# Kernel tuning notes

Measured on AMD Instinct MI355X. Metric: run time of the kernel, lower is better.

The kernel has to match this reference:

```python
import jax, jax.numpy as jnp
import numpy as np

N, E, R = 50000, 320000, 3
IN, HID, OUT = 768, 256, 64
NEG_SLOPE = 0.2


def _rgat_conv(x, src, dst, edge_type, W, q, k, bias):
    # x: [N, HID]; W: [R, HID, HID]; q,k: [HID, 1]; bias: [HID]
    n = x.shape[0]
    xw = jnp.einsum('nc,rco->rno', x, W)          # [R, N, HID] per-relation transform
    out_i = xw[edge_type, dst]                      # [E, HID] transformed target feats
    out_j = xw[edge_type, src]                      # [E, HID] transformed source feats
    alpha = jax.nn.leaky_relu(out_i @ q + out_j @ k, NEG_SLOPE)  # [E, 1]
    # across-relation segment softmax over destination nodes (PyG softmax semantics)
    m = jax.ops.segment_max(alpha, dst, num_segments=n)          # [N, 1]
    ea = jnp.exp(alpha - m[dst])
    denom = jax.ops.segment_sum(ea, dst, num_segments=n)         # [N, 1]
    a = ea / (denom[dst] + 1e-16)                                # [E, 1]
    out = jax.ops.segment_sum(a * out_j, dst, num_segments=n)    # [N, HID]
    return out + bias


def setup_inputs() -> dict:
    key = jax.random.key(0)
    ks = jax.random.split(key, 16)
    g = lambda k, shape, fan: (jax.random.normal(k, shape, jnp.float32) / np.float32(np.sqrt(fan)))
    return {
        'x': jax.random.normal(ks[0], (N, IN), jnp.float32),
        'edge_index': jax.random.randint(ks[1], (2, E), 0, N),
        'edge_type': jax.random.randint(ks[2], (E,), 0, R),
        'w_in': g(ks[3], (IN, HID), IN), 'b_in': jnp.zeros((HID,), jnp.float32),
        'conv1_w': g(ks[4], (R, HID, HID), HID),
        'conv1_q': g(ks[5], (HID, 1), HID),
        'conv1_k': g(ks[6], (HID, 1), HID),
        'conv1_b': jnp.zeros((HID,), jnp.float32),
        'conv2_w': g(ks[7], (R, HID, HID), HID),
        'conv2_q': g(ks[8], (HID, 1), HID),
        'conv2_k': g(ks[9], (HID, 1), HID),
        'conv2_b': jnp.zeros((HID,), jnp.float32),
        'w_out': g(ks[10], (HID, OUT), HID), 'b_out': jnp.zeros((OUT,), jnp.float32),
        'w_cls': g(ks[11], (OUT, 2), OUT), 'b_cls': jnp.zeros((2,), jnp.float32),
    }


def reference(x, edge_index, edge_type, w_in, b_in,
              conv1_w, conv1_q, conv1_k, conv1_b,
              conv2_w, conv2_q, conv2_k, conv2_b,
              w_out, b_out, w_cls, b_cls):
    src, dst = edge_index[0], edge_index[1]
    h = jax.nn.relu(x @ w_in + b_in)                                  # [N, HID]
    h = _rgat_conv(h, src, dst, edge_type, conv1_w, conv1_q, conv1_k, conv1_b)
    h = _rgat_conv(h, src, dst, edge_type, conv2_w, conv2_q, conv2_k, conv2_b)
    h = jax.nn.relu(h @ w_out + b_out)                                # [N, OUT]
    return h @ w_cls + b_cls                                          # [N, 2]
```

## Files before the change

### kernel.cpp

```cpp
#include <hip/hip_runtime.h>
#include <hip/hip_bf16.h>

#define RG86_NN 50000
#define RG86_NE 320000
#define RG86_NR 3
#define RG86_DIN 768
#define RG86_HID 256
#define RG86_OUT 64

typedef __bf16 rg_bv8 __attribute__((ext_vector_type(8)));
typedef short rg_sv8 __attribute__((ext_vector_type(8)));
typedef float rg_fv4 __attribute__((ext_vector_type(4)));
typedef unsigned int rg_u32;

static __device__ float rg_b2f(unsigned short u) {
  return __uint_as_float(((unsigned int)u) << 16);
}
static __device__ unsigned short rg_f2b(float f) {
  unsigned int u = __float_as_uint(f);
  u += 0x7FFFu + ((u >> 16) & 1u);
  return (unsigned short)(u >> 16);
}

static __device__ __forceinline__ void rg_gl16(const void* g, void* lds_wave_base) {
  __builtin_amdgcn_global_load_lds(
      (const __attribute__((address_space(1))) rg_u32*)(unsigned long long)(uintptr_t)g,
      (__attribute__((address_space(3))) rg_u32*)(unsigned int)(uintptr_t)lds_wave_base,
      16, 0, 0);
}

__global__ void RGATModel_86371792322702_kernel() {}

__global__ void rg_castT(const float* in, unsigned short* out, int rows, int cols) {
  int i = blockIdx.x * 256 + threadIdx.x;
  if (i < rows * cols) {
    int r = i / cols, c = i % cols;
    out[(size_t)c * rows + r] = rg_f2b(in[i]);
  }
}

__global__ void rg_castT3(const float* in, unsigned short* out) {
  int i = blockIdx.x * 256 + threadIdx.x;
  if (i < RG86_NR * RG86_HID * RG86_HID) {
    int r = i >> 16, j = i & 65535;
    int row = j >> 8, col = j & 255;
    out[(r << 16) + (col << 8) + row] = rg_f2b(in[i]);
  }
}

__global__ void rg_wqk(const float* W, const float* q, const float* k,
                       float* wq, float* wk) {
  int lane = threadIdx.x & 63;
  int p = blockIdx.x * 4 + (threadIdx.x >> 6);
  if (p >= RG86_NR * RG86_HID) return;
  const float* wr = W + (size_t)p * RG86_HID;
  float qv = 0.f, kv = 0.f;
  for (int j = lane; j < RG86_HID; j += 64) {
    float w = wr[j];
    qv += w * q[j];
    kv += w * k[j];
  }
  for (int o = 32; o >= 1; o >>= 1) { qv += __shfl_xor(qv, o); kv += __shfl_xor(kv, o); }
  if (lane == 0) { wq[p] = qv; wk[p] = kv; }
}

__global__ void rg_qk2(const unsigned short* h, const float* wq, const float* wk,
                       float* qd, float* kd) {
  int lane = threadIdx.x & 63;
  int n = blockIdx.x * 4 + (threadIdx.x >> 6);
  if (n >= RG86_NN) return;
  ushort4 hv = *(const ushort4*)(h + (size_t)n * RG86_HID + lane * 4);
  float h0 = rg_b2f(hv.x), h1 = rg_b2f(hv.y), h2 = rg_b2f(hv.z), h3 = rg_b2f(hv.w);
  float acc[6];
#pragma unroll
  for (int r = 0; r < RG86_NR; r++) {
    const float* wqr = wq + r * RG86_HID + lane * 4;
    const float* wkr = wk + r * RG86_HID + lane * 4;
    acc[r] = h0 * wqr[0] + h1 * wqr[1] + h2 * wqr[2] + h3 * wqr[3];
    acc[3 + r] = h0 * wkr[0] + h1 * wkr[1] + h2 * wkr[2] + h3 * wkr[3];
  }
#pragma unroll
  for (int j = 0; j < 6; j++)
    for (int o = 32; o >= 1; o >>= 1) acc[j] += __shfl_xor(acc[j], o);
  if (lane == 0) {
#pragma unroll
    for (int r = 0; r < RG86_NR; r++) {
      qd[r * RG86_NN + n] = acc[r];
      kd[r * RG86_NN + n] = acc[3 + r];
    }
  }
}

__global__ __launch_bounds__(256) void rg_gemm2(
    const unsigned short* A, const unsigned short* Bt, const float* bias,
    unsigned short* C, int M, int N, int K, int relu, int split) {
  __shared__ unsigned short sA[128 * 64];
  __shared__ unsigned short sB[64 * 64];
  int tid = threadIdx.x;
  int wv = tid >> 6, lane = tid & 63;
  int nwg = gridDim.x;
  int q = nwg >> 3, rres = nwg & 7;
  int xcd = blockIdx.x & 7, jj = blockIdx.x >> 3;
  int wg = (xcd < rres ? xcd * (q + 1) : rres * (q + 1) + (xcd - rres) * q) + jj;
  int ntiles = N >> 6;
  int mt = wg / ntiles, nt = wg - mt * ntiles;
  int m0 = mt * 128, n0 = nt * 64;
  int frow = lane & 15, fhi = lane >> 4;
  rg_fv4 acc[2][4] = {};
  for (int k0 = 0; k0 < K; k0 += 64) {
#pragma unroll
    for (int i = 0; i < 4; i++) {
      int idx = i * 256 + tid;
      int r = idx >> 3, s = idx & 7;
      int gr = m0 + r;
      if (gr >= M) gr = M - 1;
      const unsigned short* gp = A + (size_t)gr * K + k0 + ((s ^ (r & 7)) << 3);
      rg_gl16(gp, (char*)sA + (size_t)(i * 256 + wv * 64) * 16);
    }
#pragma unroll
    for (int i = 0; i < 2; i++) {
      int idx = i * 256 + tid;
      int r = idx >> 3, s = idx & 7;
      const unsigned short* gp = Bt + (size_t)(n0 + r) * K + k0 + ((s ^ (r & 7)) << 3);
      rg_gl16(gp, (char*)sB + (size_t)(i * 256 + wv * 64) * 16);
    }
    __syncthreads();
#pragma unroll
    for (int ks = 0; ks < 2; ks++) {
      rg_bv8 af[2], bf[4];
#pragma unroll
      for (int mf = 0; mf < 2; mf++) {
        int r = wv * 32 + mf * 16 + frow;
        int slot = (ks * 4 + fhi) ^ (r & 7);
        af[mf] = *(const rg_bv8*)((const char*)sA + r * 128 + slot * 16);
      }
#pragma unroll
      for (int nf = 0; nf < 4; nf++) {
        int r = nf * 16 + frow;
        int slot = (ks * 4 + fhi) ^ (r & 7);
        bf[nf] = *(const rg_bv8*)((const char*)sB + r * 128 + slot * 16);
      }
#pragma unroll
      for (int mf = 0; mf < 2; mf++)
#pragma unroll
        for (int nf = 0; nf < 4; nf++)
          acc[mf][nf] = __builtin_amdgcn_mfma_f32_16x16x32_bf16(af[mf], bf[nf],
                                                                acc[mf][nf], 0, 0, 0);
    }
    __syncthreads();
  }
#pragma unroll
  for (int mf = 0; mf < 2; mf++) {
#pragma unroll
    for (int nf = 0; nf < 4; nf++) {
      int col = n0 + nf * 16 + frow;
      float bv = bias ? bias[col] : 0.f;
#pragma unroll
      for (int r = 0; r < 4; r++) {
        int row = m0 + wv * 32 + mf * 16 + fhi * 4 + r;
        if (row < M) {
          float v = acc[mf][nf][r] + bv;
          if (relu && v < 0.f) v = 0.f;
          if (split)
            C[((size_t)(col >> 8) * RG86_NN + row) * 256 + (col & 255)] = rg_f2b(v);
          else
            C[(size_t)row * N + col] = rg_f2b(v);
        }
      }
    }
  }
}

__global__ __launch_bounds__(256) void rg_gemm2f(
    const float* A, const unsigned short* Bt, const float* bias,
    unsigned short* C, int M, int N, int K, int relu) {
  __shared__ unsigned short sA[128 * 64];
  __shared__ unsigned short sB[64 * 64];
  int tid = threadIdx.x;
  int wv = tid >> 6, lane = tid & 63;
  int nwg = gridDim.x;
  int q = nwg >> 3, rres = nwg & 7;
  int xcd = blockIdx.x & 7, jj = blockIdx.x >> 3;
  int wg = (xcd < rres ? xcd * (q + 1) : rres * (q + 1) + (xcd - rres) * q) + jj;
  int ntiles = N >> 6;
  int mt = wg / ntiles, nt = wg - mt * ntiles;
  int m0 = mt * 128, n0 = nt * 64;
  int frow = lane & 15, fhi = lane >> 4;
  rg_fv4 acc[2][4] = {};
  for (int k0 = 0; k0 < K; k0 += 64) {
#pragma unroll
    for (int i = 0; i < 2; i++) {
      int idx = i * 256 + tid;
      int r = idx >> 3, s = idx & 7;
      const unsigned short* gp = Bt + (size_t)(n0 + r) * K + k0 + ((s ^ (r & 7)) << 3);
      rg_gl16(gp, (char*)sB + (size_t)(i * 256 + wv * 64) * 16);
    }
    float4 fa[4][2];
#pragma unroll
    for (int i = 0; i < 4; i++) {
      int idx = i * 256 + tid;
      int r = idx >> 3, s = idx & 7;
      int gr = m0 + r;
      if (gr >= M) gr = M - 1;
      const float* gp = A + (size_t)gr * K + k0 + ((s ^ (r & 7)) << 3);
      fa[i][0] = *(const float4*)gp;
      fa[i][1] = *(const float4*)(gp + 4);
    }
#pragma unroll
    for (int i = 0; i < 4; i++) {
      int idx = i * 256 + tid;
      rg_sv8 bvv;
      bvv[0] = (short)rg_f2b(fa[i][0].x);
      bvv[1] = (short)rg_f2b(fa[i][0].y);
      bvv[2] = (short)rg_f2b(fa[i][0].z);
      bvv[3] = (short)rg_f2b(fa[i][0].w);
      bvv[4] = (short)rg_f2b(fa[i][1].x);
      bvv[5] = (short)rg_f2b(fa[i][1].y);
      bvv[6] = (short)rg_f2b(fa[i][1].z);
      bvv[7] = (short)rg_f2b(fa[i][1].w);
      *(rg_sv8*)((char*)sA + (size_t)idx * 16) = bvv;
    }
    __syncthreads();
#pragma unroll
    for (int ks = 0; ks < 2; ks++) {
      rg_bv8 af[2], bf[4];
#pragma unroll
      for (int mf = 0; mf < 2; mf++) {
        int r = wv * 32 + mf * 16 + frow;
        int slot = (ks * 4 + fhi) ^ (r & 7);
        af[mf] = *(const rg_bv8*)((const char*)sA + r * 128 + slot * 16);
      }
#pragma unroll
      for (int nf = 0; nf < 4; nf++) {
        int r = nf * 16 + frow;
        int slot = (ks * 4 + fhi) ^ (r & 7);
        bf[nf] = *(const rg_bv8*)((const char*)sB + r * 128 + slot * 16);
      }
#pragma unroll
      for (int mf = 0; mf < 2; mf++)
#pragma unroll
        for (int nf = 0; nf < 4; nf++)
          acc[mf][nf] = __builtin_amdgcn_mfma_f32_16x16x32_bf16(af[mf], bf[nf],
                                                                acc[mf][nf], 0, 0, 0);
    }
    __syncthreads();
  }
#pragma unroll
  for (int mf = 0; mf < 2; mf++) {
#pragma unroll
    for (int nf = 0; nf < 4; nf++) {
      int col = n0 + nf * 16 + frow;
      float bv = bias ? bias[col] : 0.f;
#pragma unroll
      for (int r = 0; r < 4; r++) {
        int row = m0 + wv * 32 + mf * 16 + fhi * 4 + r;
        if (row < M) {
          float v = acc[mf][nf][r] + bv;
          if (relu && v < 0.f) v = 0.f;
          C[(size_t)row * N + col] = rg_f2b(v);
        }
      }
    }
  }
}

__global__ void rg_hist(const int* d, int* counts) {
  int e = blockIdx.x * 256 + threadIdx.x;
  if (e < RG86_NE) atomicAdd(&counts[d[e]], 1);
}

__global__ void rg_scan1(const int* counts, int* tmp, int* bsum, int n) {
  int b = blockIdx.x, t = threadIdx.x;
  int base = b * 1024 + t * 4;
  int v0 = 0, v1 = 0, v2 = 0, v3 = 0;
  if (base + 3 < n) {
    int4 v = *(const int4*)(counts + base);
    v0 = v.x; v1 = v.y; v2 = v.z; v3 = v.w;
  } else {
    if (base + 0 < n) v0 = counts[base + 0];
    if (base + 1 < n) v1 = counts[base + 1];
    if (base + 2 < n) v2 = counts[base + 2];
    if (base + 3 < n) v3 = counts[base + 3];
  }
  int tsum = v0 + v1 + v2 + v3;
  int lane = t & 63, wave = t >> 6;
  int s = tsum;
  for (int off = 1; off < 64; off <<= 1) {
    int u = __shfl_up(s, off);
    if (lane >= off) s += u;
  }
  __shared__ int wsum[4];
  if (lane == 63) wsum[wave] = s;
  __syncthreads();
  int woff = 0;
  for (int w = 0; w < wave; w++) woff += wsum[w];
  int excl = woff + s - tsum;
  int e0 = excl, e1 = e0 + v0, e2 = e1 + v1, e3 = e2 + v2;
  if (base + 3 < n) {
    *(int4*)(tmp + base) = make_int4(e0, e1, e2, e3);
  } else {
    if (base + 0 < n) tmp[base + 0] = e0;
    if (base + 1 < n) tmp[base + 1] = e1;
    if (base + 2 < n) tmp[base + 2] = e2;
    if (base + 3 < n) tmp[base + 3] = e3;
  }
  if (t == 255) bsum[b] = woff + s;
}

__global__ void rg_scan2(int* bsum, int* rowptr, int nb, int n) {
  int lane = threadIdx.x;
  int v = (lane < nb) ? bsum[lane] : 0;
  int s = v;
  for (int off = 1; off < 64; off <<= 1) {
    int u = __shfl_up(s, off);
    if (lane >= off) s += u;
  }
  if (lane < nb) bsum[lane] = s - v;
  if (lane == 63) rowptr[n] = s;
}

__global__ void rg_scan3(const int* bsum, int* rowptr, int* cursor, int n) {
  int b = blockIdx.x, t = threadIdx.x;
  int base = b * 1024 + t * 4;
  int off = bsum[b];
  if (base + 3 < n) {
    int4 v = *(const int4*)(cursor + base);
    int4 o = make_int4(v.x + off, v.y + off, v.z + off, v.w + off);
    *(int4*)(rowptr + base) = o;
    *(int4*)(cursor + base) = o;
  } else {
    for (int j = 0; j < 4; j++)
      if (base + j < n) {
        int o = cursor[base + j] + off;
        rowptr[base + j] = o;
        cursor[base + j] = o;
      }
  }
}

__global__ void rg_scatter(const int* d, int* cursor, int* perm) {
  int e = blockIdx.x * 256 + threadIdx.x;
  if (e < RG86_NE) perm[atomicAdd(&cursor[d[e]], 1)] = e;
}

__global__ void rg_edge(const int* perm, const int* src, const int* dst,
                        const int* et, const float* qd, const float* kd,
                        float* alphap, int* srcrel) {
  int i = blockIdx.x * 256 + threadIdx.x;
  if (i >= RG86_NE) return;
  int e = perm[i];
  int t = et[e], sv = src[e], dv = dst[e];
  float al = qd[t * RG86_NN + dv] + kd[t * RG86_NN + sv];
  al = al > 0.f ? al : 0.2f * al;
  alphap[i] = al;
  srcrel[i] = t * RG86_NN + sv;
}

__global__ void rg_agg(const int* rowptr, const float* alphap, const int* srcrel,
                       const unsigned short* xw, const float* bias,
                       unsigned short* out) {
  __shared__ float sw[4][64];
  __shared__ int ssrc[4][64];
  int lane = threadIdx.x & 63;
  int wv = threadIdx.x >> 6;
  int node = blockIdx.x * 4 + wv;
  if (node >= RG86_NN) return;
  int s0 = rowptr[node], s1 = rowptr[node + 1];
  int c0 = lane * 4;
  float a0 = 0.f, a1 = 0.f, a2 = 0.f, a3 = 0.f;
  if (s1 > s0) {
    float m = -1e30f;
    for (int bs = s0; bs < s1; bs += 64) {
      int i = bs + lane;
      float al = (i < s1) ? alphap[i] : -1e30f;
      m = fmaxf(m, al);
    }
    for (int o = 32; o >= 1; o >>= 1) m = fmaxf(m, __shfl_xor(m, o));
    float den = 0.f;
    for (int bs = s0; bs < s1; bs += 64) {
      int i = bs + lane;
      if (i < s1) den += __expf(alphap[i] - m);
    }
    for (int o = 32; o >= 1; o >>= 1) den += __shfl_xor(den, o);
    float inv = 1.f / (den + 1e-16f);
    for (int bs = s0; bs < s1; bs += 64) {
      int i = bs + lane;
      int nch = s1 - bs; if (nch > 64) nch = 64;
      float w = 0.f; int sr = 0;
      if (i < s1) { w = __expf(alphap[i] - m) * inv; sr = srcrel[i]; }
      sw[wv][lane] = w;
      ssrc[wv][lane] = sr;
#pragma unroll 4
      for (int j = 0; j < nch; j++) {
        float wj = sw[wv][j];
        ushort4 v = *(const ushort4*)(xw + (size_t)ssrc[wv][j] * RG86_HID + c0);
        a0 += wj * rg_b2f(v.x);
        a1 += wj * rg_b2f(v.y);
        a2 += wj * rg_b2f(v.z);
        a3 += wj * rg_b2f(v.w);
      }
    }
  }
  unsigned short* op = out + (size_t)node * RG86_HID + c0;
  op[0] = rg_f2b(a0 + bias[c0 + 0]);
  op[1] = rg_f2b(a1 + bias[c0 + 1]);
  op[2] = rg_f2b(a2 + bias[c0 + 2]);
  op[3] = rg_f2b(a3 + bias[c0 + 3]);
}

__global__ void rg_cls(const unsigned short* h4, const float* wc, const float* bc,
                       float* out) {
  int n = blockIdx.x * 256 + threadIdx.x;
  if (n >= RG86_NN) return;
  float a0 = bc[0], a1 = bc[1];
  const unsigned short* hr = h4 + (size_t)n * RG86_OUT;
  for (int j = 0; j < RG86_OUT; j++) {
    float h = rg_b2f(hr[j]);
    a0 += h * wc[j * 2 + 0];
    a1 += h * wc[j * 2 + 1];
  }
  out[n * 2 + 0] = a0;
  out[n * 2 + 1] = a1;
}

extern "C" void kernel_launch(void* const* d_in, const int* in_sizes, int n_in,
                              void* d_out, int out_size, void* d_ws, size_t ws_size,
                              hipStream_t stream) {
  (void)in_sizes; (void)n_in; (void)out_size;
  const float* x = (const float*)d_in[0];
  const int* ei = (const int*)d_in[1];
  const int* etp = (const int*)d_in[2];
  const float* w_in = (const float*)d_in[3];
  const float* b_in = (const float*)d_in[4];
  const float* c1w = (const float*)d_in[5];
  const float* c1q = (const float*)d_in[6];
  const float* c1k = (const float*)d_in[7];
  const float* c1b = (const float*)d_in[8];
  const float* c2w = (const float*)d_in[9];
  const float* c2q = (const float*)d_in[10];
  const float* c2k = (const float*)d_in[11];
  const float* c2b = (const float*)d_in[12];
  const float* w_out = (const float*)d_in[13];
  const float* b_out = (const float*)d_in[14];
  const float* w_cls = (const float*)d_in[15];
  const float* b_cls = (const float*)d_in[16];
  const int* esrc = ei;
  const int* edst = ei + RG86_NE;

  char* base = (char*)d_ws;
  size_t off = 0;
  unsigned short* xw = (unsigned short*)(base + off);
  off += (size_t)RG86_NR * RG86_NN * RG86_HID * 2;
  unsigned short* h1b = (unsigned short*)(base + off); off += (size_t)RG86_NN * RG86_HID * 2;
  unsigned short* h2b = (unsigned short*)(base + off); off += (size_t)RG86_NN * RG86_HID * 2;
  unsigned short* h4b = (unsigned short*)(base + off); off += (size_t)RG86_NN * RG86_OUT * 2;
  unsigned short* w_inT = (unsigned short*)(base + off); off += (size_t)RG86_DIN * RG86_HID * 2;
  unsigned short* c1wT = (unsigned short*)(base + off); off += (size_t)RG86_NR * RG86_HID * RG86_HID * 2;
  unsigned short* c2wT = (unsigned short*)(base + off); off += (size_t)RG86_NR * RG86_HID * RG86_HID * 2;
  unsigned short* w_outT = (unsigned short*)(base + off); off += (size_t)RG86_HID * RG86_OUT * 2;
  float* qd = (float*)(base + off); off += (size_t)RG86_NR * RG86_NN * 4;
  float* kd = (float*)(base + off); off += (size_t)RG86_NR * RG86_NN * 4;
  float* wq1 = (float*)(base + off); off += (size_t)RG86_NR * RG86_HID * 4;
  float* wk1 = (float*)(base + off); off += (size_t)RG86_NR * RG86_HID * 4;
  float* wq2 = (float*)(base + off); off += (size_t)RG86_NR * RG86_HID * 4;
  float* wk2 = (float*)(base + off); off += (size_t)RG86_NR * RG86_HID * 4;
  int* counts = (int*)(base + off); off += (size_t)RG86_NN * 4;
  int* rowptr = (int*)(base + off); off += (size_t)(RG86_NN + 4) * 4;
  int* cursor = (int*)(base + off); off += (size_t)RG86_NN * 4;
  int* perm = (int*)(base + off); off += (size_t)RG86_NE * 4;
  int* bsum = (int*)(base + off); off += (size_t)64 * 4;
  float* alphap = (float*)(base + off); off += (size_t)RG86_NE * 4;
  int* srcrel = (int*)(base + off); off += (size_t)RG86_NE * 4;
  if (off > ws_size) return;

  int mt128 = (RG86_NN + 127) / 128;
  int nsb = (RG86_NN + 1023) / 1024;

  rg_castT<<<(RG86_DIN * RG86_HID + 255) / 256, 256, 0, stream>>>(
      w_in, w_inT, RG86_DIN, RG86_HID);
  rg_castT3<<<(RG86_NR * RG86_HID * RG86_HID + 255) / 256, 256, 0, stream>>>(c1w, c1wT);
  rg_castT3<<<(RG86_NR * RG86_HID * RG86_HID + 255) / 256, 256, 0, stream>>>(c2w, c2wT);
  rg_castT<<<(RG86_HID * RG86_OUT + 255) / 256, 256, 0, stream>>>(
      w_out, w_outT, RG86_HID, RG86_OUT);
  rg_wqk<<<(RG86_NR * RG86_HID + 3) / 4, 256, 0, stream>>>(c1w, c1q, c1k, wq1, wk1);
  rg_wqk<<<(RG86_NR * RG86_HID + 3) / 4, 256, 0, stream>>>(c2w, c2q, c2k, wq2, wk2);

  rg_gemm2f<<<mt128 * 4, 256, 0, stream>>>(x, w_inT, b_in, h1b,
                                           RG86_NN, RG86_HID, RG86_DIN, 1);

  hipMemsetAsync(counts, 0, (size_t)RG86_NN * 4, stream);
  rg_hist<<<(RG86_NE + 255) / 256, 256, 0, stream>>>(edst, counts);
  rg_scan1<<<nsb, 256, 0, stream>>>(counts, cursor, bsum, RG86_NN);
  rg_scan2<<<1, 64, 0, stream>>>(bsum, rowptr, nsb, RG86_NN);
  rg_scan3<<<nsb, 256, 0, stream>>>(bsum, rowptr, cursor, RG86_NN);
  rg_scatter<<<(RG86_NE + 255) / 256, 256, 0, stream>>>(edst, cursor, perm);

  rg_gemm2<<<mt128 * 12, 256, 0, stream>>>(h1b, c1wT, (const float*)0, xw,
                                           RG86_NN, RG86_NR * RG86_HID, RG86_HID, 0, 1);
  rg_qk2<<<(RG86_NN + 3) / 4, 256, 0, stream>>>(h1b, wq1, wk1, qd, kd);
  rg_edge<<<(RG86_NE + 255) / 256, 256, 0, stream>>>(perm, esrc, edst, etp, qd, kd,
                                                     alphap, srcrel);
  rg_agg<<<(RG86_NN + 3) / 4, 256, 0, stream>>>(rowptr, alphap, srcrel,
                                                xw, c1b, h2b);

  rg_gemm2<<<mt128 * 12, 256, 0, stream>>>(h2b, c2wT, (const float*)0, xw,
                                           RG86_NN, RG86_NR * RG86_HID, RG86_HID, 0, 1);
  rg_qk2<<<(RG86_NN + 3) / 4, 256, 0, stream>>>(h2b, wq2, wk2, qd, kd);
  rg_edge<<<(RG86_NE + 255) / 256, 256, 0, stream>>>(perm, esrc, edst, etp, qd, kd,
                                                     alphap, srcrel);
  rg_agg<<<(RG86_NN + 3) / 4, 256, 0, stream>>>(rowptr, alphap, srcrel,
                                                xw, c2b, h1b);

  rg_gemm2<<<mt128, 256, 0, stream>>>(h1b, w_outT, b_out, h4b,
                                      RG86_NN, RG86_OUT, RG86_HID, 1, 0);

  rg_cls<<<(RG86_NN + 255) / 256, 256, 0, stream>>>(h4b, w_cls, b_cls, (float*)d_out);
}
```

Before: 622.7 us.

## Widen GEMM tiles to 128x128, pre-cast input to bf16, fuse classifier into output GEMM

The GEMM N-tile grows from 64 to 128 columns, so each A tile loaded into LDS feeds twice as many MFMAs and the grid shrinks by half. The fp32 input x is first cast to bf16 in a separate vectorized pass, so the input GEMM can use the async global_load_lds path instead of converting inside its loop. The final w_out GEMM now applies relu and the 64x2 classifier in its epilogue with a shuffle reduction, removing the h4 buffer and the rg_cls kernel. The cost is an extra full read and write of x for the cast, plus more accumulator registers that may reduce occupancy.

```diff
diff --git a/kernel.cpp b/kernel.cpp
--- a/kernel.cpp
+++ b/kernel.cpp
@@ -30,6 +30,15 @@
 }
 
 __global__ void RGATModel_86371792322702_kernel() {}
+
+__global__ void rg_cast(const float* in, unsigned short* out, int n) {
+  int i = (blockIdx.x * 256 + threadIdx.x) * 4;
+  if (i < n) {
+    float4 v = *(const float4*)(in + i);
+    ushort4 o = make_ushort4(rg_f2b(v.x), rg_f2b(v.y), rg_f2b(v.z), rg_f2b(v.w));
+    *(ushort4*)(out + i) = o;
+  }
+}
 
 __global__ void rg_castT(const float* in, unsigned short* out, int rows, int cols) {
   int i = blockIdx.x * 256 + threadIdx.x;
@@ -91,22 +100,22 @@
   }
 }
 
-__global__ __launch_bounds__(256) void rg_gemm2(
+__global__ __launch_bounds__(256) void rg_gemm2w(
     const unsigned short* A, const unsigned short* Bt, const float* bias,
     unsigned short* C, int M, int N, int K, int relu, int split) {
   __shared__ unsigned short sA[128 * 64];
-  __shared__ unsigned short sB[64 * 64];
+  __shared__ unsigned short sB[128 * 64];
   int tid = threadIdx.x;
   int wv = tid >> 6, lane = tid & 63;
   int nwg = gridDim.x;
   int q = nwg >> 3, rres = nwg & 7;
   int xcd = blockIdx.x & 7, jj = blockIdx.x >> 3;
   int wg = (xcd < rres ? xcd * (q + 1) : rres * (q + 1) + (xcd - rres) * q) + jj;
-  int ntiles = N >> 6;
+  int ntiles = N >> 7;
   int mt = wg / ntiles, nt = wg - mt * ntiles;
-  int m0 = mt * 128, n0 = nt * 64;
+  int m0 = mt * 128, n0 = nt * 128;
   int frow = lane & 15, fhi = lane >> 4;
-  rg_fv4 acc[2][4] = {};
+  rg_fv4 acc[2][8] = {};
   for (int k0 = 0; k0 < K; k0 += 64) {
 #pragma unroll
     for (int i = 0; i < 4; i++) {
@@ -118,7 +127,7 @@
       rg_gl16(gp, (char*)sA + (size_t)(i * 256 + wv * 64) * 16);
     }
 #pragma unroll
-    for (int i = 0; i < 2; i++) {
+    for (int i = 0; i < 4; i++) {
       int idx = i * 256 + tid;
       int r = idx >> 3, s = idx & 7;
       const unsigned short* gp = Bt + (size_t)(n0 + r) * K + k0 + ((s ^ (r & 7)) << 3);
@@ -127,7 +136,7 @@
     __syncthreads();
 #pragma unroll
     for (int ks = 0; ks < 2; ks++) {
-      rg_bv8 af[2], bf[4];
+      rg_bv8 af[2], bf[8];
 #pragma unroll
       for (int mf = 0; mf < 2; mf++) {
         int r = wv * 32 + mf * 16 + frow;
@@ -135,7 +144,7 @@
         af[mf] = *(const rg_bv8*)((const char*)sA + r * 128 + slot * 16);
       }
 #pragma unroll
-      for (int nf = 0; nf < 4; nf++) {
+      for (int nf = 0; nf < 8; nf++) {
         int r = nf * 16 + frow;
         int slot = (ks * 4 + fhi) ^ (r & 7);
         bf[nf] = *(const rg_bv8*)((const char*)sB + r * 128 + slot * 16);
@@ -143,7 +152,7 @@
 #pragma unroll
       for (int mf = 0; mf < 2; mf++)
 #pragma unroll
-        for (int nf = 0; nf < 4; nf++)
+        for (int nf = 0; nf < 8; nf++)
           acc[mf][nf] = __builtin_amdgcn_mfma_f32_16x16x32_bf16(af[mf], bf[nf],
                                                                 acc[mf][nf], 0, 0, 0);
     }
@@ -152,7 +161,7 @@
 #pragma unroll
   for (int mf = 0; mf < 2; mf++) {
 #pragma unroll
-    for (int nf = 0; nf < 4; nf++) {
+    for (int nf = 0; nf < 8; nf++) {
       int col = n0 + nf * 16 + frow;
       float bv = bias ? bias[col] : 0.f;
 #pragma unroll
@@ -171,54 +180,33 @@
   }
 }
 
-__global__ __launch_bounds__(256) void rg_gemm2f(
-    const float* A, const unsigned short* Bt, const float* bias,
-    unsigned short* C, int M, int N, int K, int relu) {
+__global__ __launch_bounds__(256) void rg_gemm2c(
+    const unsigned short* A, const unsigned short* Bt, const float* bias,
+    const float* wc, const float* bc, float* out, int M, int K) {
   __shared__ unsigned short sA[128 * 64];
   __shared__ unsigned short sB[64 * 64];
   int tid = threadIdx.x;
   int wv = tid >> 6, lane = tid & 63;
-  int nwg = gridDim.x;
-  int q = nwg >> 3, rres = nwg & 7;
-  int xcd = blockIdx.x & 7, jj = blockIdx.x >> 3;
-  int wg = (xcd < rres ? xcd * (q + 1) : rres * (q + 1) + (xcd - rres) * q) + jj;
-  int ntiles = N >> 6;
-  int mt = wg / ntiles, nt = wg - mt * ntiles;
-  int m0 = mt * 128, n0 = nt * 64;
+  int mt = blockIdx.x;
+  int m0 = mt * 128;
   int frow = lane & 15, fhi = lane >> 4;
   rg_fv4 acc[2][4] = {};
   for (int k0 = 0; k0 < K; k0 += 64) {
-#pragma unroll
-    for (int i = 0; i < 2; i++) {
-      int idx = i * 256 + tid;
-      int r = idx >> 3, s = idx & 7;
-      const unsigned short* gp = Bt + (size_t)(n0 + r) * K + k0 + ((s ^ (r & 7)) << 3);
-      rg_gl16(gp, (char*)sB + (size_t)(i * 256 + wv * 64) * 16);
-    }
-    float4 fa[4][2];
 #pragma unroll
     for (int i = 0; i < 4; i++) {
       int idx = i * 256 + tid;
       int r = idx >> 3, s = idx & 7;
       int gr = m0 + r;
       if (gr >= M) gr = M - 1;
-      const float* gp = A + (size_t)gr * K + k0 + ((s ^ (r & 7)) << 3);
-      fa[i][0] = *(const float4*)gp;
-      fa[i][1] = *(const float4*)(gp + 4);
-    }
-#pragma unroll
-    for (int i = 0; i < 4; i++) {
+      const unsigned short* gp = A + (size_t)gr * K + k0 + ((s ^ (r & 7)) << 3);
+      rg_gl16(gp, (char*)sA + (size_t)(i * 256 + wv * 64) * 16);
+    }
+#pragma unroll
+    for (int i = 0; i < 2; i++) {
       int idx = i * 256 + tid;
-      rg_sv8 bvv;
-      bvv[0] = (short)rg_f2b(fa[i][0].x);
-      bvv[1] = (short)rg_f2b(fa[i][0].y);
-      bvv[2] = (short)rg_f2b(fa[i][0].z);
-      bvv[3] = (short)rg_f2b(fa[i][0].w);
-      bvv[4] = (short)rg_f2b(fa[i][1].x);
-      bvv[5] = (short)rg_f2b(fa[i][1].y);
-      bvv[6] = (short)rg_f2b(fa[i][1].z);
-      bvv[7] = (short)rg_f2b(fa[i][1].w);
-      *(rg_sv8*)((char*)sA + (size_t)idx * 16) = bvv;
+      int r = idx >> 3, s = idx & 7;
+      const unsigned short* gp = Bt + (size_t)r * K + k0 + ((s ^ (r & 7)) << 3);
+      rg_gl16(gp, (char*)sB + (size_t)(i * 256 + wv * 64) * 16);
     }
     __syncthreads();
 #pragma unroll
@@ -245,20 +233,29 @@
     }
     __syncthreads();
   }
+  float bc0 = bc[0], bc1 = bc[1];
 #pragma unroll
   for (int mf = 0; mf < 2; mf++) {
 #pragma unroll
-    for (int nf = 0; nf < 4; nf++) {
-      int col = n0 + nf * 16 + frow;
-      float bv = bias ? bias[col] : 0.f;
-#pragma unroll
-      for (int r = 0; r < 4; r++) {
-        int row = m0 + wv * 32 + mf * 16 + fhi * 4 + r;
-        if (row < M) {
-          float v = acc[mf][nf][r] + bv;
-          if (relu && v < 0.f) v = 0.f;
-          C[(size_t)row * N + col] = rg_f2b(v);
-        }
+    for (int r = 0; r < 4; r++) {
+      float p0 = 0.f, p1 = 0.f;
+#pragma unroll
+      for (int nf = 0; nf < 4; nf++) {
+        int col = nf * 16 + frow;
+        float v = acc[mf][nf][r] + bias[col];
+        if (v < 0.f) v = 0.f;
+        p0 += v * wc[col * 2 + 0];
+        p1 += v * wc[col * 2 + 1];
+      }
+#pragma unroll
+      for (int o = 1; o < 16; o <<= 1) {
+        p0 += __shfl_xor(p0, o);
+        p1 += __shfl_xor(p1, o);
+      }
+      int row = m0 + wv * 32 + mf * 16 + fhi * 4 + r;
+      if (frow == 0 && row < M) {
+        out[row * 2 + 0] = p0 + bc0;
+        out[row * 2 + 1] = p1 + bc1;
       }
     }
   }
@@ -406,21 +403,6 @@
   op[1] = rg_f2b(a1 + bias[c0 + 1]);
   op[2] = rg_f2b(a2 + bias[c0 + 2]);
   op[3] = rg_f2b(a3 + bias[c0 + 3]);
-}
-
-__global__ void rg_cls(const unsigned short* h4, const float* wc, const float* bc,
-                       float* out) {
-  int n = blockIdx.x * 256 + threadIdx.x;
-  if (n >= RG86_NN) return;
-  float a0 = bc[0], a1 = bc[1];
-  const unsigned short* hr = h4 + (size_t)n * RG86_OUT;
-  for (int j = 0; j < RG86_OUT; j++) {
-    float h = rg_b2f(hr[j]);
-    a0 += h * wc[j * 2 + 0];
-    a1 += h * wc[j * 2 + 1];
-  }
-  out[n * 2 + 0] = a0;
-  out[n * 2 + 1] = a1;
 }
 
 extern "C" void kernel_launch(void* const* d_in, const int* in_sizes, int n_in,
@@ -449,11 +431,11 @@
 
   char* base = (char*)d_ws;
   size_t off = 0;
-  unsigned short* xw = (unsigned short*)(base + off);
-  off += (size_t)RG86_NR * RG86_NN * RG86_HID * 2;
+  unsigned short* xb = (unsigned short*)(base + off);
+  unsigned short* xw = xb;
+  off += (size_t)RG86_NN * RG86_DIN * 2;
   unsigned short* h1b = (unsigned short*)(base + off); off += (size_t)RG86_NN * RG86_HID * 2;
   unsigned short* h2b = (unsigned short*)(base + off); off += (size_t)RG86_NN * RG86_HID * 2;
-  unsigned short* h4b = (unsigned short*)(base + off); off += (size_t)RG86_NN * RG86_OUT * 2;
   unsigned short* w_inT = (unsigned short*)(base + off); off += (size_t)RG86_DIN * RG86_HID * 2;
   unsigned short* c1wT = (unsigned short*)(base + off); off += (size_t)RG86_NR * RG86_HID * RG86_HID * 2;
   unsigned short* c2wT = (unsigned short*)(base + off); off += (size_t)RG86_NR * RG86_HID * RG86_HID * 2;
@@ -476,6 +458,8 @@
   int mt128 = (RG86_NN + 127) / 128;
   int nsb = (RG86_NN + 1023) / 1024;
 
+  rg_cast<<<(RG86_NN * RG86_DIN / 4 + 255) / 256, 256, 0, stream>>>(
+      x, xb, RG86_NN * RG86_DIN);
   rg_castT<<<(RG86_DIN * RG86_HID + 255) / 256, 256, 0, stream>>>(
       w_in, w_inT, RG86_DIN, RG86_HID);
   rg_castT3<<<(RG86_NR * RG86_HID * RG86_HID + 255) / 256, 256, 0, stream>>>(c1w, c1wT);
@@ -485,8 +469,8 @@
   rg_wqk<<<(RG86_NR * RG86_HID + 3) / 4, 256, 0, stream>>>(c1w, c1q, c1k, wq1, wk1);
   rg_wqk<<<(RG86_NR * RG86_HID + 3) / 4, 256, 0, stream>>>(c2w, c2q, c2k, wq2, wk2);
 
-  rg_gemm2f<<<mt128 * 4, 256, 0, stream>>>(x, w_inT, b_in, h1b,
-                                           RG86_NN, RG86_HID, RG86_DIN, 1);
+  rg_gemm2w<<<mt128 * 2, 256, 0, stream>>>(xb, w_inT, b_in, h1b,
+                                           RG86_NN, RG86_HID, RG86_DIN, 1, 0);
 
   hipMemsetAsync(counts, 0, (size_t)RG86_NN * 4, stream);
   rg_hist<<<(RG86_NE + 255) / 256, 256, 0, stream>>>(edst, counts);
@@ -495,7 +479,7 @@
   rg_scan3<<<nsb, 256, 0, stream>>>(bsum, rowptr, cursor, RG86_NN);
   rg_scatter<<<(RG86_NE + 255) / 256, 256, 0, stream>>>(edst, cursor, perm);
 
-  rg_gemm2<<<mt128 * 12, 256, 0, stream>>>(h1b, c1wT, (const float*)0, xw,
+  rg_gemm2w<<<mt128 * 6, 256, 0, stream>>>(h1b, c1wT, (const float*)0, xw,
                                            RG86_NN, RG86_NR * RG86_HID, RG86_HID, 0, 1);
   rg_qk2<<<(RG86_NN + 3) / 4, 256, 0, stream>>>(h1b, wq1, wk1, qd, kd);
   rg_edge<<<(RG86_NE + 255) / 256, 256, 0, stream>>>(perm, esrc, edst, etp, qd, kd,
@@ -503,7 +487,7 @@
   rg_agg<<<(RG86_NN + 3) / 4, 256, 0, stream>>>(rowptr, alphap, srcrel,
                                                 xw, c1b, h2b);
 
-  rg_gemm2<<<mt128 * 12, 256, 0, stream>>>(h2b, c2wT, (const float*)0, xw,
+  rg_gemm2w<<<mt128 * 6, 256, 0, stream>>>(h2b, c2wT, (const float*)0, xw,
                                            RG86_NN, RG86_NR * RG86_HID, RG86_HID, 0, 1);
   rg_qk2<<<(RG86_NN + 3) / 4, 256, 0, stream>>>(h2b, wq2, wk2, qd, kd);
   rg_edge<<<(RG86_NE + 255) / 256, 256, 0, stream>>>(perm, esrc, edst, etp, qd, kd,
@@ -511,8 +495,6 @@
   rg_agg<<<(RG86_NN + 3) / 4, 256, 0, stream>>>(rowptr, alphap, srcrel,
                                                 xw, c2b, h1b);
 
-  rg_gemm2<<<mt128, 256, 0, stream>>>(h1b, w_outT, b_out, h4b,
-                                      RG86_NN, RG86_OUT, RG86_HID, 1, 0);
-
-  rg_cls<<<(RG86_NN + 255) / 256, 256, 0, stream>>>(h4b, w_cls, b_cls, (float*)d_out);
-}
+  rg_gemm2c<<<mt128, 256, 0, stream>>>(h1b, w_outT, b_out, w_cls, b_cls,
+                                       (float*)d_out, RG86_NN, RG86_HID);
+}
```

Result: slower. 668.8 us (+7.4%).
